# Optimization experiments

Measured on AMD Instinct MI355X. Metric: run time of the kernel, lower is better.

The kernel has to match this reference:

```python
import jax, jax.numpy as jnp
import numpy as np

D_MODEL = 512
NUM_HEADS = 8
HEAD_DIM = D_MODEL // NUM_HEADS
NUM_Z_BINS = 16
MAX_Z = 5.0
N = 2048


def setup_inputs() -> dict:
    key = jax.random.key(0)
    ks = jax.random.split(key, 12)
    s = 1.0 / np.sqrt(D_MODEL)
    return {
        "x": jax.random.normal(ks[0], (N, D_MODEL), dtype=jnp.float32),
        "z_matrix": jax.random.uniform(ks[1], (N, N), dtype=jnp.float32),
        "Wq": jax.random.normal(ks[2], (D_MODEL, D_MODEL), dtype=jnp.float32) * s,
        "bq": jnp.zeros((D_MODEL,), dtype=jnp.float32),
        "Wk": jax.random.normal(ks[3], (D_MODEL, D_MODEL), dtype=jnp.float32) * s,
        "bk": jnp.zeros((D_MODEL,), dtype=jnp.float32),
        "Wv": jax.random.normal(ks[4], (D_MODEL, D_MODEL), dtype=jnp.float32) * s,
        "bv": jnp.zeros((D_MODEL,), dtype=jnp.float32),
        "Wo": jax.random.normal(ks[5], (D_MODEL, D_MODEL), dtype=jnp.float32) * s,
        "bo": jnp.zeros((D_MODEL,), dtype=jnp.float32),
        "z_table": jax.random.normal(ks[6], (NUM_Z_BINS, NUM_HEADS), dtype=jnp.float32) * 0.02,
    }


def reference(x, z_matrix, Wq, bq, Wk, bk, Wv, bv, Wo, bo, z_table):
    n = x.shape[0]
    scale = HEAD_DIM ** -0.5
    q = (x @ Wq + bq).reshape(n, NUM_HEADS, HEAD_DIM)
    k = (x @ Wk + bk).reshape(n, NUM_HEADS, HEAD_DIM)
    v = (x @ Wv + bv).reshape(n, NUM_HEADS, HEAD_DIM)
    # [n, h, m] attention scores
    scores = jnp.einsum('nhd,mhd->nhm', q, k) * scale
    # Z-bus relative bias: bin pairwise z values into NUM_Z_BINS over [0, MAX_Z],
    # look up per-head bias from the embedding table.
    bins = jnp.clip(jnp.floor(z_matrix / MAX_Z * NUM_Z_BINS).astype(jnp.int32), 0, NUM_Z_BINS - 1)
    bias = z_table[bins]                    # [n, n, h]
    scores = scores + jnp.transpose(bias, (0, 2, 1))  # [n, h, n]
    attn = jax.nn.softmax(scores, axis=-1)  # dropout p=0.0 (eval)
    out = jnp.einsum('nhm,mhd->nhd', attn, v).reshape(n, D_MODEL)
    return out @ Wo + bo
```

## Files before the change

kernel.cpp:

```cpp
#include <hip/hip_runtime.h>


#define NTOK   2048
#define DM     512
#define NH     8
#define DH     64
#define NBINS  16
#define NSPLIT 4
#define KPS    (NTOK / NSPLIT)

typedef float  f32x16 __attribute__((ext_vector_type(16)));
typedef short  short8 __attribute__((ext_vector_type(8)));
typedef unsigned short ushort_t;

#define MFMA32(A, B, C) __builtin_amdgcn_mfma_f32_32x32x16_bf16((A), (B), (C), 0, 0, 0)

__device__ __forceinline__ unsigned short f2bf(float x) {
    union { float f; unsigned u; } v; v.f = x;
    unsigned r = v.u + 0x7FFFu + ((v.u >> 16) & 1u);
    return (unsigned short)(r >> 16);
}
__device__ __forceinline__ float bf2f(unsigned short b) {
    union { unsigned u; float f; } v; v.u = ((unsigned)b) << 16;
    return v.f;
}
__device__ __forceinline__ void splitbf(float x, unsigned short& hi, unsigned short& lo) {
    hi = f2bf(x);
    lo = f2bf(x - bf2f(hi));
}

union FragU { unsigned u[4]; short8 s; };

__device__ __forceinline__ int z_to_bin(float z) {
    int b = (int)floorf(z / 5.0f * 16.0f);
    return b < 0 ? 0 : (b > 15 ? 15 : b);
}

__global__ __launch_bounds__(256)
void bins_kernel(const float* __restrict__ z, unsigned char* __restrict__ bins) {
    int i = (blockIdx.x * 256 + threadIdx.x) * 4;
    float4 zv = *reinterpret_cast<const float4*>(z + i);
    uchar4 b;
    b.x = (unsigned char)z_to_bin(zv.x);
    b.y = (unsigned char)z_to_bin(zv.y);
    b.z = (unsigned char)z_to_bin(zv.z);
    b.w = (unsigned char)z_to_bin(zv.w);
    *reinterpret_cast<uchar4*>(bins + i) = b;
}

__global__ __launch_bounds__(256)
void prep_w(const float* __restrict__ Wq, const float* __restrict__ Wk,
            const float* __restrict__ Wv, const float* __restrict__ Wo,
            ushort_t* __restrict__ wt_hi_base, ushort_t* __restrict__ wt_lo_base) {
    const int z = blockIdx.z;
    const float* __restrict__ W = z == 0 ? Wq : z == 1 ? Wk : z == 2 ? Wv : Wo;
    ushort_t* __restrict__ th = wt_hi_base + (size_t)z * DM * DM * 2;
    ushort_t* __restrict__ tl = wt_lo_base + (size_t)z * DM * DM * 2;

    const int r0 = blockIdx.y * 32;
    const int c0 = blockIdx.x * 32;
    const int t  = threadIdx.x;

    __shared__ float Tl[32][33];

    {
        const int r = t >> 3, c4 = (t & 7) * 4;
        float4 v = *reinterpret_cast<const float4*>(W + (size_t)(r0 + r) * DM + c0 + c4);
        Tl[r][c4 + 0] = v.x; Tl[r][c4 + 1] = v.y; Tl[r][c4 + 2] = v.z; Tl[r][c4 + 3] = v.w;
    }
    __syncthreads();
    {
        const int c = t >> 3, r4 = (t & 7) * 4;
        ushort_t h4[4], l4[4];
        #pragma unroll
        for (int k = 0; k < 4; ++k) splitbf(Tl[r4 + k][c], h4[k], l4[k]);
        *reinterpret_cast<ushort4*>(th + (size_t)(c0 + c) * DM + r0 + r4) =
            make_ushort4(h4[0], h4[1], h4[2], h4[3]);
        *reinterpret_cast<ushort4*>(tl + (size_t)(c0 + c) * DM + r0 + r4) =
            make_ushort4(l4[0], l4[1], l4[2], l4[3]);
    }
}

__global__ __launch_bounds__(256)
void conv_x(const float* __restrict__ x, ushort_t* __restrict__ xh, ushort_t* __restrict__ xl) {
    int i = (blockIdx.x * 256 + threadIdx.x) * 4;
    float4 v = *reinterpret_cast<const float4*>(x + i);
    ushort_t h[4], l[4];
    splitbf(v.x, h[0], l[0]); splitbf(v.y, h[1], l[1]);
    splitbf(v.z, h[2], l[2]); splitbf(v.w, h[3], l[3]);
    *reinterpret_cast<ushort4*>(xh + i) = make_ushort4(h[0], h[1], h[2], h[3]);
    *reinterpret_cast<ushort4*>(xl + i) = make_ushort4(l[0], l[1], l[2], l[3]);
}

__global__ __launch_bounds__(256, 3)
void qkv_gemm_mfma(const ushort_t* __restrict__ x_hi, const ushort_t* __restrict__ x_lo,
                   const ushort_t* __restrict__ wqt_hi, const ushort_t* __restrict__ wqt_lo,
                   const ushort_t* __restrict__ wkt_hi, const ushort_t* __restrict__ wkt_lo,
                   const ushort_t* __restrict__ wvt_hi, const ushort_t* __restrict__ wvt_lo,
                   const float* __restrict__ bq, const float* __restrict__ bk,
                   const float* __restrict__ bv,
                   ushort_t* __restrict__ q_hi, ushort_t* __restrict__ q_lo,
                   ushort_t* __restrict__ k_hi, ushort_t* __restrict__ k_lo,
                   ushort_t* __restrict__ vT_hi, ushort_t* __restrict__ vT_lo) {
    const int z = blockIdx.z;
    const ushort_t* __restrict__ bt_hi = z == 0 ? wqt_hi : z == 1 ? wkt_hi : wvt_hi;
    const ushort_t* __restrict__ bt_lo = z == 0 ? wqt_lo : z == 1 ? wkt_lo : wvt_lo;
    const float*    __restrict__ bias  = z == 0 ? bq : z == 1 ? bk : bv;

    const int n0 = blockIdx.x * 64;
    const int m0 = blockIdx.y * 64;
    const int t  = threadIdx.x;
    const int wid = t >> 6, l = t & 63, hf = l >> 5, lq = l & 31;
    const int wm = wid >> 1, wn = wid & 1;

    __shared__ __align__(16) ushort_t Ash_hi[64 * 40], Ash_lo[64 * 40];
    __shared__ __align__(16) ushort_t Bsh_hi[64 * 40], Bsh_lo[64 * 40];

    f32x16 acc;
    #pragma unroll
    for (int i = 0; i < 16; ++i) acc[i] = 0.0f;

    const int sr = t >> 2, sc = t & 3;

    for (int k0 = 0; k0 < DM; k0 += 32) {
        __syncthreads();
        *reinterpret_cast<uint4*>(&Ash_hi[sr * 40 + 8 * sc]) =
            *reinterpret_cast<const uint4*>(&x_hi[(size_t)(m0 + sr) * DM + k0 + 8 * sc]);
        *reinterpret_cast<uint4*>(&Ash_lo[sr * 40 + 8 * sc]) =
            *reinterpret_cast<const uint4*>(&x_lo[(size_t)(m0 + sr) * DM + k0 + 8 * sc]);
        *reinterpret_cast<uint4*>(&Bsh_hi[sr * 40 + 8 * sc]) =
            *reinterpret_cast<const uint4*>(&bt_hi[(size_t)(n0 + sr) * DM + k0 + 8 * sc]);
        *reinterpret_cast<uint4*>(&Bsh_lo[sr * 40 + 8 * sc]) =
            *reinterpret_cast<const uint4*>(&bt_lo[(size_t)(n0 + sr) * DM + k0 + 8 * sc]);
        __syncthreads();

        #pragma unroll
        for (int kp = 0; kp < 2; ++kp) {
            const int co = 8 * (hf + 2 * kp);
            short8 ah = *reinterpret_cast<const short8*>(&Ash_hi[(32 * wm + lq) * 40 + co]);
            short8 al = *reinterpret_cast<const short8*>(&Ash_lo[(32 * wm + lq) * 40 + co]);
            short8 bh = *reinterpret_cast<const short8*>(&Bsh_hi[(32 * wn + lq) * 40 + co]);
            short8 bl = *reinterpret_cast<const short8*>(&Bsh_lo[(32 * wn + lq) * 40 + co]);
            acc = MFMA32(ah, bh, acc);
            acc = MFMA32(ah, bl, acc);
            acc = MFMA32(al, bh, acc);
        }
    }

    const int nl = lq + 32 * wn;
    const float bval = bias[n0 + nl];
    const int hh = n0 >> 6;

    #pragma unroll
    for (int r = 0; r < 16; ++r) {
        const int ml = (r & 3) + 8 * (r >> 2) + 4 * hf + 32 * wm;
        const float v = acc[r] + bval;
        ushort_t hi, lo; splitbf(v, hi, lo);
        if (z < 2) {
            ushort_t* dh = z == 0 ? q_hi : k_hi;
            ushort_t* dl = z == 0 ? q_lo : k_lo;
            const size_t o = ((size_t)hh * NTOK + m0 + ml) * DH + nl;
            dh[o] = hi; dl[o] = lo;
        } else {
            const size_t o = ((size_t)hh * DH + nl) * NTOK + m0 + ml;
            vT_hi[o] = hi; vT_lo[o] = lo;
        }
    }
}

__global__ __launch_bounds__(256, 3)
void wo_gemm_mfma(const ushort_t* __restrict__ a_hi, const ushort_t* __restrict__ a_lo,
                  const ushort_t* __restrict__ bt_hi, const ushort_t* __restrict__ bt_lo,
                  const float* __restrict__ bias, float* __restrict__ out) {
    const int n0 = blockIdx.x * 64;
    const int m0 = blockIdx.y * 64;
    const int t  = threadIdx.x;
    const int wid = t >> 6, l = t & 63, hf = l >> 5, lq = l & 31;
    const int wm = wid >> 1, wn = wid & 1;

    __shared__ __align__(16) ushort_t Ash_hi[64 * 40], Ash_lo[64 * 40];
    __shared__ __align__(16) ushort_t Bsh_hi[64 * 40], Bsh_lo[64 * 40];

    f32x16 acc;
    #pragma unroll
    for (int i = 0; i < 16; ++i) acc[i] = 0.0f;

    const int sr = t >> 2, sc = t & 3;

    for (int k0 = 0; k0 < DM; k0 += 32) {
        __syncthreads();
        *reinterpret_cast<uint4*>(&Ash_hi[sr * 40 + 8 * sc]) =
            *reinterpret_cast<const uint4*>(&a_hi[(size_t)(m0 + sr) * DM + k0 + 8 * sc]);
        *reinterpret_cast<uint4*>(&Ash_lo[sr * 40 + 8 * sc]) =
            *reinterpret_cast<const uint4*>(&a_lo[(size_t)(m0 + sr) * DM + k0 + 8 * sc]);
        *reinterpret_cast<uint4*>(&Bsh_hi[sr * 40 + 8 * sc]) =
            *reinterpret_cast<const uint4*>(&bt_hi[(size_t)(n0 + sr) * DM + k0 + 8 * sc]);
        *reinterpret_cast<uint4*>(&Bsh_lo[sr * 40 + 8 * sc]) =
            *reinterpret_cast<const uint4*>(&bt_lo[(size_t)(n0 + sr) * DM + k0 + 8 * sc]);
        __syncthreads();

        #pragma unroll
        for (int kp = 0; kp < 2; ++kp) {
            const int co = 8 * (hf + 2 * kp);
            short8 ah = *reinterpret_cast<const short8*>(&Ash_hi[(32 * wm + lq) * 40 + co]);
            short8 al = *reinterpret_cast<const short8*>(&Ash_lo[(32 * wm + lq) * 40 + co]);
            short8 bh = *reinterpret_cast<const short8*>(&Bsh_hi[(32 * wn + lq) * 40 + co]);
            short8 bl = *reinterpret_cast<const short8*>(&Bsh_lo[(32 * wn + lq) * 40 + co]);
            acc = MFMA32(ah, bh, acc);
            acc = MFMA32(ah, bl, acc);
            acc = MFMA32(al, bh, acc);
        }
    }

    const int nl = lq + 32 * wn;
    const float bval = bias[n0 + nl];
    #pragma unroll
    for (int r = 0; r < 16; ++r) {
        const int ml = (r & 3) + 8 * (r >> 2) + 4 * hf + 32 * wm;
        out[(size_t)(m0 + ml) * DM + n0 + nl] = acc[r] + bval;
    }
}

__global__ __launch_bounds__(256, 2)
void attn_mfma(const ushort_t* __restrict__ q_hi, const ushort_t* __restrict__ q_lo,
               const ushort_t* __restrict__ k_hi, const ushort_t* __restrict__ k_lo,
               const ushort_t* __restrict__ vT_hi, const ushort_t* __restrict__ vT_lo,
               const unsigned char* __restrict__ bins_g, const float* __restrict__ z_table,
               float* __restrict__ po, float* __restrict__ pm, float* __restrict__ pl) {
    const int hd = blockIdx.y;
    const int q0 = blockIdx.x * 128;
    const int zs = blockIdx.z;
    const int t  = threadIdx.x;
    const int wid = t >> 6, l = t & 63, hf = l >> 5, lq = l & 31;
    const int qs = q0 + 32 * wid;

    __shared__ __align__(16) ushort_t Ksh_hi[64 * 72], Ksh_lo[64 * 72];
    __shared__ __align__(16) ushort_t Vsh_hi[64 * 72], Vsh_lo[64 * 72];
    __shared__ __align__(16) unsigned char Bsh[128 * 80];

    const float ztab = z_table[(l & 15) * NH + hd];

    short8 qf_hi[4], qf_lo[4];
    #pragma unroll
    for (int kp = 0; kp < 4; ++kp) {
        const size_t o = ((size_t)hd * NTOK + qs + lq) * DH + 8 * hf + 16 * kp;
        qf_hi[kp] = *reinterpret_cast<const short8*>(&q_hi[o]);
        qf_lo[kp] = *reinterpret_cast<const short8*>(&q_lo[o]);
    }

    float m_run = -1e30f, l_run = 0.0f;
    f32x16 oacc0, oacc1;
    #pragma unroll
    for (int i = 0; i < 16; ++i) { oacc0[i] = 0.0f; oacc1[i] = 0.0f; }

    const float scale = 0.125f;
    const int kbase = zs * KPS;

    for (int kt8 = 0; kt8 < KPS / 64; ++kt8) {
        const int ktb = kbase + kt8 * 64;
        __syncthreads();
        #pragma unroll
        for (int i = 0; i < 2; ++i) {
            const int idx = t + 256 * i;
            const int r = idx >> 3, c = idx & 7;
            const size_t kg = ((size_t)hd * NTOK + ktb + r) * DH + 8 * c;
            const size_t vg = ((size_t)hd * DH + r) * NTOK + ktb + 8 * c;
            *reinterpret_cast<uint4*>(&Ksh_hi[r * 72 + 8 * c]) =
                *reinterpret_cast<const uint4*>(&k_hi[kg]);
            *reinterpret_cast<uint4*>(&Ksh_lo[r * 72 + 8 * c]) =
                *reinterpret_cast<const uint4*>(&k_lo[kg]);
            *reinterpret_cast<uint4*>(&Vsh_hi[r * 72 + 8 * c]) =
                *reinterpret_cast<const uint4*>(&vT_hi[vg]);
            *reinterpret_cast<uint4*>(&Vsh_lo[r * 72 + 8 * c]) =
                *reinterpret_cast<const uint4*>(&vT_lo[vg]);
        }
        #pragma unroll
        for (int i = 0; i < 2; ++i) {
            const int idx = t + 256 * i;
            const int qr = idx >> 2, c = idx & 3;
            *reinterpret_cast<uint4*>(&Bsh[qr * 80 + 16 * c]) =
                *reinterpret_cast<const uint4*>(&bins_g[(size_t)(q0 + qr) * NTOK + ktb + 16 * c]);
        }
        __syncthreads();

        f32x16 sacc0, sacc1;
        #pragma unroll
        for (int i = 0; i < 16; ++i) { sacc0[i] = 0.0f; sacc1[i] = 0.0f; }
        #pragma unroll
        for (int kp = 0; kp < 4; ++kp) {
            const int co = 8 * (hf + 2 * kp);
            short8 k0h = *reinterpret_cast<const short8*>(&Ksh_hi[lq * 72 + co]);
            short8 k0l = *reinterpret_cast<const short8*>(&Ksh_lo[lq * 72 + co]);
            short8 k1h = *reinterpret_cast<const short8*>(&Ksh_hi[(lq + 32) * 72 + co]);
            short8 k1l = *reinterpret_cast<const short8*>(&Ksh_lo[(lq + 32) * 72 + co]);
            sacc0 = MFMA32(k0h, qf_hi[kp], sacc0);
            sacc0 = MFMA32(k0h, qf_lo[kp], sacc0);
            sacc0 = MFMA32(k0l, qf_hi[kp], sacc0);
            sacc1 = MFMA32(k1h, qf_hi[kp], sacc1);
            sacc1 = MFMA32(k1h, qf_lo[kp], sacc1);
            sacc1 = MFMA32(k1l, qf_hi[kp], sacc1);
        }

        float sv[2][16];
        #pragma unroll
        for (int t2 = 0; t2 < 2; ++t2) {
            #pragma unroll
            for (int b = 0; b < 4; ++b) {
                const unsigned bw = *reinterpret_cast<const unsigned*>(
                    &Bsh[(32 * wid + lq) * 80 + 4 * (hf + 2 * b + 8 * t2)]);
                #pragma unroll
                for (int c = 0; c < 4; ++c) {
                    const int r = c + 4 * b;
                    const int src = (int)((bw >> (8 * c)) & 0xFF) | (l & 48);
                    const float bias = __shfl(ztab, src, 64);
                    const float sraw = (t2 == 0 ? sacc0[r] : sacc1[r]);
                    sv[t2][r] = sraw * scale + bias;
                }
            }
        }

        float tm = sv[0][0];
        #pragma unroll
        for (int t2 = 0; t2 < 2; ++t2)
            #pragma unroll
            for (int r = 0; r < 16; ++r) tm = fmaxf(tm, sv[t2][r]);
        tm = fmaxf(tm, __shfl_xor(tm, 32, 64));
        const float mn = fmaxf(m_run, tm);
        const float ef = __expf(m_run - mn);
        m_run = mn;

        float pv[2][16];
        float ts = 0.0f;
        #pragma unroll
        for (int t2 = 0; t2 < 2; ++t2)
            #pragma unroll
            for (int r = 0; r < 16; ++r) {
                const float p = __expf(sv[t2][r] - mn);
                pv[t2][r] = p;
                ts += p;
            }
        ts += __shfl_xor(ts, 32, 64);
        l_run = l_run * ef + ts;

        #pragma unroll
        for (int r = 0; r < 16; ++r) {
            const int qloc = (r & 3) + 8 * (r >> 2) + 4 * hf;
            const float efr = __shfl(ef, qloc | (l & 32), 64);
            oacc0[r] *= efr;
            oacc1[r] *= efr;
        }

        unsigned phi[2][8], plo[2][8];
        #pragma unroll
        for (int t2 = 0; t2 < 2; ++t2)
            #pragma unroll
            for (int i = 0; i < 8; ++i) {
                ushort_t ha, la, hb, lb;
                splitbf(pv[t2][2 * i],     ha, la);
                splitbf(pv[t2][2 * i + 1], hb, lb);
                phi[t2][i] = (unsigned)ha | ((unsigned)hb << 16);
                plo[t2][i] = (unsigned)la | ((unsigned)lb << 16);
            }

        FragU paf_hi[2][2], paf_lo[2][2];
        #pragma unroll
        for (int t2 = 0; t2 < 2; ++t2)
            #pragma unroll
            for (int e = 0; e < 2; ++e) {
                {
                    const unsigned pA0 = phi[t2][4 * e], pA1 = phi[t2][4 * e + 1];
                    const unsigned pB0 = phi[t2][4 * e + 2], pB1 = phi[t2][4 * e + 3];
                    const unsigned s0 = hf ? pA0 : pB0, s1 = hf ? pA1 : pB1;
                    const unsigned r0 = (unsigned)__shfl_xor((int)s0, 32, 64);
                    const unsigned r1 = (unsigned)__shfl_xor((int)s1, 32, 64);
                    paf_hi[t2][e].u[0] = hf ? r0 : pA0;
                    paf_hi[t2][e].u[1] = hf ? r1 : pA1;
                    paf_hi[t2][e].u[2] = hf ? pB0 : r0;
                    paf_hi[t2][e].u[3] = hf ? pB1 : r1;
                }
                {
                    const unsigned pA0 = plo[t2][4 * e], pA1 = plo[t2][4 * e + 1];
                    const unsigned pB0 = plo[t2][4 * e + 2], pB1 = plo[t2][4 * e + 3];
                    const unsigned s0 = hf ? pA0 : pB0, s1 = hf ? pA1 : pB1;
                    const unsigned r0 = (unsigned)__shfl_xor((int)s0, 32, 64);
                    const unsigned r1 = (unsigned)__shfl_xor((int)s1, 32, 64);
                    paf_lo[t2][e].u[0] = hf ? r0 : pA0;
                    paf_lo[t2][e].u[1] = hf ? r1 : pA1;
                    paf_lo[t2][e].u[2] = hf ? pB0 : r0;
                    paf_lo[t2][e].u[3] = hf ? pB1 : r1;
                }
            }

        #pragma unroll
        for (int kp = 0; kp < 4; ++kp) {
            const int t2 = kp >> 1, e = kp & 1;
            const int co = 8 * (hf + 2 * kp);
            short8 v0h = *reinterpret_cast<const short8*>(&Vsh_hi[lq * 72 + co]);
            short8 v0l = *reinterpret_cast<const short8*>(&Vsh_lo[lq * 72 + co]);
            oacc0 = MFMA32(paf_hi[t2][e].s, v0h, oacc0);
            oacc0 = MFMA32(paf_hi[t2][e].s, v0l, oacc0);
            oacc0 = MFMA32(paf_lo[t2][e].s, v0h, oacc0);
            short8 v1h = *reinterpret_cast<const short8*>(&Vsh_hi[(lq + 32) * 72 + co]);
            short8 v1l = *reinterpret_cast<const short8*>(&Vsh_lo[(lq + 32) * 72 + co]);
            oacc1 = MFMA32(paf_hi[t2][e].s, v1h, oacc1);
            oacc1 = MFMA32(paf_hi[t2][e].s, v1l, oacc1);
            oacc1 = MFMA32(paf_lo[t2][e].s, v1h, oacc1);
        }
    }

    #pragma unroll
    for (int r = 0; r < 16; ++r) {
        const int qloc = (r & 3) + 8 * (r >> 2) + 4 * hf;
        const size_t row = ((size_t)(zs * NH + hd) * NTOK + qs + qloc) * DH;
        po[row + lq]      = oacc0[r];
        po[row + lq + 32] = oacc1[r];
    }
    if (hf == 0) {
        const size_t row = (size_t)(zs * NH + hd) * NTOK + qs + lq;
        pm[row] = m_run;
        pl[row] = l_run;
    }
}

__global__ __launch_bounds__(256)
void merge_kernel(const float* __restrict__ po, const float* __restrict__ pm,
                  const float* __restrict__ pl,
                  ushort_t* __restrict__ o_hi, ushort_t* __restrict__ o_lo) {
    const int idx = blockIdx.x * 256 + threadIdx.x;
    const int d4 = (idx & 15) * 4;
    const int q  = (idx >> 4) & (NTOK - 1);
    const int hh = idx >> 15;

    float ms[NSPLIT];
    float M = -1e30f;
    #pragma unroll
    for (int s = 0; s < NSPLIT; ++s) {
        ms[s] = pm[((size_t)s * NH + hh) * NTOK + q];
        M = fmaxf(M, ms[s]);
    }
    float L = 0.0f;
    float4 o = make_float4(0.f, 0.f, 0.f, 0.f);
    #pragma unroll
    for (int s = 0; s < NSPLIT; ++s) {
        const float w = __expf(ms[s] - M);
        L += w * pl[((size_t)s * NH + hh) * NTOK + q];
        float4 p = *reinterpret_cast<const float4*>(
            po + (((size_t)s * NH + hh) * NTOK + q) * DH + d4);
        o.x += w * p.x; o.y += w * p.y; o.z += w * p.z; o.w += w * p.w;
    }
    const float inv = 1.0f / L;
    o.x *= inv; o.y *= inv; o.z *= inv; o.w *= inv;

    ushort_t h4[4], l4[4];
    splitbf(o.x, h4[0], l4[0]); splitbf(o.y, h4[1], l4[1]);
    splitbf(o.z, h4[2], l4[2]); splitbf(o.w, h4[3], l4[3]);
    const size_t oo = (size_t)q * DM + hh * DH + d4;
    *reinterpret_cast<ushort4*>(o_hi + oo) = make_ushort4(h4[0], h4[1], h4[2], h4[3]);
    *reinterpret_cast<ushort4*>(o_lo + oo) = make_ushort4(l4[0], l4[1], l4[2], l4[3]);
}

extern "C" void kernel_launch(void* const* d_in, const int* in_sizes, int n_in,
                              void* d_out, int out_size, void* d_ws, size_t ws_size,
                              hipStream_t stream) {
    const float* x        = (const float*)d_in[0];
    const float* z_matrix = (const float*)d_in[1];
    const float* Wq       = (const float*)d_in[2];
    const float* bq       = (const float*)d_in[3];
    const float* Wk       = (const float*)d_in[4];
    const float* bk       = (const float*)d_in[5];
    const float* Wv       = (const float*)d_in[6];
    const float* bv       = (const float*)d_in[7];
    const float* Wo       = (const float*)d_in[8];
    const float* bo       = (const float*)d_in[9];
    const float* z_table  = (const float*)d_in[10];
    float* out            = (float*)d_out;

    uint8_t* w = (uint8_t*)d_ws;
    const size_t MB = 1024 * 1024;
    ushort_t* x_hi  = (ushort_t*)(w + 0);
    ushort_t* x_lo  = (ushort_t*)(w + 2  * MB);
    ushort_t* wqt_hi= (ushort_t*)(w + 4  * MB);
    ushort_t* wqt_lo= (ushort_t*)(w + 4  * MB + 512 * 1024);
    ushort_t* wkt_hi= (ushort_t*)(w + 5  * MB);
    ushort_t* wkt_lo= (ushort_t*)(w + 5  * MB + 512 * 1024);
    ushort_t* wvt_hi= (ushort_t*)(w + 6  * MB);
    ushort_t* wvt_lo= (ushort_t*)(w + 6  * MB + 512 * 1024);
    ushort_t* wot_hi= (ushort_t*)(w + 7  * MB);
    ushort_t* wot_lo= (ushort_t*)(w + 7  * MB + 512 * 1024);
    ushort_t* q_hi  = (ushort_t*)(w + 8  * MB);
    ushort_t* q_lo  = (ushort_t*)(w + 10 * MB);
    ushort_t* k_hi  = (ushort_t*)(w + 12 * MB);
    ushort_t* k_lo  = (ushort_t*)(w + 14 * MB);
    ushort_t* vT_hi = (ushort_t*)(w + 16 * MB);
    ushort_t* vT_lo = (ushort_t*)(w + 18 * MB);
    unsigned char* bins = (unsigned char*)(w + 20 * MB);
    float* po = (float*)(w + 24 * MB);
    float* pm = (float*)(w + 40 * MB);
    float* pl = (float*)(w + 40 * MB + 256 * 1024);
    ushort_t* o_hi = x_hi;
    ushort_t* o_lo = x_lo;

    bins_kernel<<<dim3(NTOK * NTOK / 4 / 256), dim3(256), 0, stream>>>(z_matrix, bins);
    prep_w<<<dim3(16, 16, 4), dim3(256), 0, stream>>>(Wq, Wk, Wv, Wo,
        (ushort_t*)(w + 4 * MB), (ushort_t*)(w + 4 * MB + 512 * 1024));
    conv_x<<<dim3(NTOK * DM / 4 / 256), dim3(256), 0, stream>>>(x, x_hi, x_lo);

    qkv_gemm_mfma<<<dim3(DM / 64, NTOK / 64, 3), dim3(256), 0, stream>>>(
        x_hi, x_lo,
        wqt_hi, wqt_lo, wkt_hi, wkt_lo, wvt_hi, wvt_lo,
        bq, bk, bv,
        q_hi, q_lo, k_hi, k_lo, vT_hi, vT_lo);

    attn_mfma<<<dim3(NTOK / 128, NH, NSPLIT), dim3(256), 0, stream>>>(
        q_hi, q_lo, k_hi, k_lo, vT_hi, vT_lo, bins, z_table, po, pm, pl);

    merge_kernel<<<dim3(NH * NTOK * DH / 4 / 256), dim3(256), 0, stream>>>(
        po, pm, pl, o_hi, o_lo);

    wo_gemm_mfma<<<dim3(DM / 64, NTOK / 64), dim3(256), 0, stream>>>(
        o_hi, o_lo, wot_hi, wot_lo, bo, out);
}
```

Measured before the change: 174.5 us.

## Prefetch tiles into registers, merge prep kernels, raise MFMA priority

Three preprocessing kernels (z binning, x split, weight transpose/split) are merged into one launch to cut launch overhead. The QKV GEMM, Wo GEMM and attention kernels now load the next K-tile into registers while MFMAs run on the current LDS tile, so global-load latency overlaps compute. MFMA sections are wrapped in s_setprio to favour matrix issue. The manual bf16 rounding is replaced with the HIP intrinsic. The prefetch adds register pressure, which could lower occupancy, especially in the attention kernel.

```diff
diff --git a/kernel.cpp b/kernel.cpp
--- a/kernel.cpp
+++ b/kernel.cpp
@@ -1,4 +1,5 @@
 #include <hip/hip_runtime.h>
+#include <hip/hip_bf16.h>
 
 
 #define NTOK   2048
@@ -15,16 +16,16 @@
 
 #define MFMA32(A, B, C) __builtin_amdgcn_mfma_f32_32x32x16_bf16((A), (B), (C), 0, 0, 0)
 
-__device__ __forceinline__ unsigned short f2bf(float x) {
-    union { float f; unsigned u; } v; v.f = x;
-    unsigned r = v.u + 0x7FFFu + ((v.u >> 16) & 1u);
-    return (unsigned short)(r >> 16);
-}
-__device__ __forceinline__ float bf2f(unsigned short b) {
+__device__ __forceinline__ ushort_t f2bf(float x) {
+    __hip_bfloat16 h = __float2bfloat16(x);
+    union { __hip_bfloat16 b; ushort_t u; } v; v.b = h;
+    return v.u;
+}
+__device__ __forceinline__ float bf2f(ushort_t b) {
     union { unsigned u; float f; } v; v.u = ((unsigned)b) << 16;
     return v.f;
 }
-__device__ __forceinline__ void splitbf(float x, unsigned short& hi, unsigned short& lo) {
+__device__ __forceinline__ void splitbf(float x, ushort_t& hi, ushort_t& lo) {
     hi = f2bf(x);
     lo = f2bf(x - bf2f(hi));
 }
@@ -37,59 +38,58 @@
 }
 
 __global__ __launch_bounds__(256)
-void bins_kernel(const float* __restrict__ z, unsigned char* __restrict__ bins) {
-    int i = (blockIdx.x * 256 + threadIdx.x) * 4;
-    float4 zv = *reinterpret_cast<const float4*>(z + i);
-    uchar4 b;
-    b.x = (unsigned char)z_to_bin(zv.x);
-    b.y = (unsigned char)z_to_bin(zv.y);
-    b.z = (unsigned char)z_to_bin(zv.z);
-    b.w = (unsigned char)z_to_bin(zv.w);
-    *reinterpret_cast<uchar4*>(bins + i) = b;
-}
-
-__global__ __launch_bounds__(256)
-void prep_w(const float* __restrict__ Wq, const float* __restrict__ Wk,
-            const float* __restrict__ Wv, const float* __restrict__ Wo,
-            ushort_t* __restrict__ wt_hi_base, ushort_t* __restrict__ wt_lo_base) {
-    const int z = blockIdx.z;
-    const float* __restrict__ W = z == 0 ? Wq : z == 1 ? Wk : z == 2 ? Wv : Wo;
-    ushort_t* __restrict__ th = wt_hi_base + (size_t)z * DM * DM * 2;
-    ushort_t* __restrict__ tl = wt_lo_base + (size_t)z * DM * DM * 2;
-
-    const int r0 = blockIdx.y * 32;
-    const int c0 = blockIdx.x * 32;
-    const int t  = threadIdx.x;
-
+void prep_all(const float* __restrict__ z, unsigned char* __restrict__ bins,
+              const float* __restrict__ x, ushort_t* __restrict__ xh, ushort_t* __restrict__ xl,
+              const float* __restrict__ Wq, const float* __restrict__ Wk,
+              const float* __restrict__ Wv, const float* __restrict__ Wo,
+              ushort_t* __restrict__ wt_hi_base, ushort_t* __restrict__ wt_lo_base) {
+    const int bid = blockIdx.x;
+    const int t   = threadIdx.x;
     __shared__ float Tl[32][33];
 
-    {
-        const int r = t >> 3, c4 = (t & 7) * 4;
-        float4 v = *reinterpret_cast<const float4*>(W + (size_t)(r0 + r) * DM + c0 + c4);
-        Tl[r][c4 + 0] = v.x; Tl[r][c4 + 1] = v.y; Tl[r][c4 + 2] = v.z; Tl[r][c4 + 3] = v.w;
-    }
-    __syncthreads();
-    {
-        const int c = t >> 3, r4 = (t & 7) * 4;
-        ushort_t h4[4], l4[4];
-        #pragma unroll
-        for (int k = 0; k < 4; ++k) splitbf(Tl[r4 + k][c], h4[k], l4[k]);
-        *reinterpret_cast<ushort4*>(th + (size_t)(c0 + c) * DM + r0 + r4) =
-            make_ushort4(h4[0], h4[1], h4[2], h4[3]);
-        *reinterpret_cast<ushort4*>(tl + (size_t)(c0 + c) * DM + r0 + r4) =
-            make_ushort4(l4[0], l4[1], l4[2], l4[3]);
-    }
-}
-
-__global__ __launch_bounds__(256)
-void conv_x(const float* __restrict__ x, ushort_t* __restrict__ xh, ushort_t* __restrict__ xl) {
-    int i = (blockIdx.x * 256 + threadIdx.x) * 4;
-    float4 v = *reinterpret_cast<const float4*>(x + i);
-    ushort_t h[4], l[4];
-    splitbf(v.x, h[0], l[0]); splitbf(v.y, h[1], l[1]);
-    splitbf(v.z, h[2], l[2]); splitbf(v.w, h[3], l[3]);
-    *reinterpret_cast<ushort4*>(xh + i) = make_ushort4(h[0], h[1], h[2], h[3]);
-    *reinterpret_cast<ushort4*>(xl + i) = make_ushort4(l[0], l[1], l[2], l[3]);
+    if (bid < 4096) {
+        int i = (bid * 256 + t) * 4;
+        float4 zv = *reinterpret_cast<const float4*>(z + i);
+        uchar4 b;
+        b.x = (unsigned char)z_to_bin(zv.x);
+        b.y = (unsigned char)z_to_bin(zv.y);
+        b.z = (unsigned char)z_to_bin(zv.z);
+        b.w = (unsigned char)z_to_bin(zv.w);
+        *reinterpret_cast<uchar4*>(bins + i) = b;
+    } else if (bid < 5120) {
+        int i = ((bid - 4096) * 256 + t) * 4;
+        float4 v = *reinterpret_cast<const float4*>(x + i);
+        ushort_t h[4], l[4];
+        splitbf(v.x, h[0], l[0]); splitbf(v.y, h[1], l[1]);
+        splitbf(v.z, h[2], l[2]); splitbf(v.w, h[3], l[3]);
+        *reinterpret_cast<ushort4*>(xh + i) = make_ushort4(h[0], h[1], h[2], h[3]);
+        *reinterpret_cast<ushort4*>(xl + i) = make_ushort4(l[0], l[1], l[2], l[3]);
+    } else {
+        const int pz  = bid - 5120;
+        const int zz  = pz >> 8;
+        const int rem = pz & 255;
+        const float* __restrict__ W = zz == 0 ? Wq : zz == 1 ? Wk : zz == 2 ? Wv : Wo;
+        ushort_t* __restrict__ th = wt_hi_base + (size_t)zz * DM * DM * 2;
+        ushort_t* __restrict__ tl = wt_lo_base + (size_t)zz * DM * DM * 2;
+        const int r0 = (rem >> 4) * 32;
+        const int c0 = (rem & 15) * 32;
+        {
+            const int r = t >> 3, c4 = (t & 7) * 4;
+            float4 v = *reinterpret_cast<const float4*>(W + (size_t)(r0 + r) * DM + c0 + c4);
+            Tl[r][c4 + 0] = v.x; Tl[r][c4 + 1] = v.y; Tl[r][c4 + 2] = v.z; Tl[r][c4 + 3] = v.w;
+        }
+        __syncthreads();
+        {
+            const int c = t >> 3, r4 = (t & 7) * 4;
+            ushort_t h4[4], l4[4];
+            #pragma unroll
+            for (int k = 0; k < 4; ++k) splitbf(Tl[r4 + k][c], h4[k], l4[k]);
+            *reinterpret_cast<ushort4*>(th + (size_t)(c0 + c) * DM + r0 + r4) =
+                make_ushort4(h4[0], h4[1], h4[2], h4[3]);
+            *reinterpret_cast<ushort4*>(tl + (size_t)(c0 + c) * DM + r0 + r4) =
+                make_ushort4(l4[0], l4[1], l4[2], l4[3]);
+        }
+    }
 }
 
 __global__ __launch_bounds__(256, 3)
@@ -122,18 +122,25 @@
 
     const int sr = t >> 2, sc = t & 3;
 
+    uint4 ra_h, ra_l, rb_h, rb_l;
+    auto LOAD = [&](int k0) {
+        ra_h = *reinterpret_cast<const uint4*>(&x_hi[(size_t)(m0 + sr) * DM + k0 + 8 * sc]);
+        ra_l = *reinterpret_cast<const uint4*>(&x_lo[(size_t)(m0 + sr) * DM + k0 + 8 * sc]);
+        rb_h = *reinterpret_cast<const uint4*>(&bt_hi[(size_t)(n0 + sr) * DM + k0 + 8 * sc]);
+        rb_l = *reinterpret_cast<const uint4*>(&bt_lo[(size_t)(n0 + sr) * DM + k0 + 8 * sc]);
+    };
+    LOAD(0);
+
     for (int k0 = 0; k0 < DM; k0 += 32) {
         __syncthreads();
-        *reinterpret_cast<uint4*>(&Ash_hi[sr * 40 + 8 * sc]) =
-            *reinterpret_cast<const uint4*>(&x_hi[(size_t)(m0 + sr) * DM + k0 + 8 * sc]);
-        *reinterpret_cast<uint4*>(&Ash_lo[sr * 40 + 8 * sc]) =
-            *reinterpret_cast<const uint4*>(&x_lo[(size_t)(m0 + sr) * DM + k0 + 8 * sc]);
-        *reinterpret_cast<uint4*>(&Bsh_hi[sr * 40 + 8 * sc]) =
-            *reinterpret_cast<const uint4*>(&bt_hi[(size_t)(n0 + sr) * DM + k0 + 8 * sc]);
-        *reinterpret_cast<uint4*>(&Bsh_lo[sr * 40 + 8 * sc]) =
-            *reinterpret_cast<const uint4*>(&bt_lo[(size_t)(n0 + sr) * DM + k0 + 8 * sc]);
-        __syncthreads();
-
+        *reinterpret_cast<uint4*>(&Ash_hi[sr * 40 + 8 * sc]) = ra_h;
+        *reinterpret_cast<uint4*>(&Ash_lo[sr * 40 + 8 * sc]) = ra_l;
+        *reinterpret_cast<uint4*>(&Bsh_hi[sr * 40 + 8 * sc]) = rb_h;
+        *reinterpret_cast<uint4*>(&Bsh_lo[sr * 40 + 8 * sc]) = rb_l;
+        __syncthreads();
+        if (k0 + 32 < DM) LOAD(k0 + 32);
+
+        __builtin_amdgcn_s_setprio(1);
         #pragma unroll
         for (int kp = 0; kp < 2; ++kp) {
             const int co = 8 * (hf + 2 * kp);
@@ -145,6 +152,7 @@
             acc = MFMA32(ah, bl, acc);
             acc = MFMA32(al, bh, acc);
         }
+        __builtin_amdgcn_s_setprio(0);
     }
 
     const int nl = lq + 32 * wn;
@@ -187,18 +195,25 @@
 
     const int sr = t >> 2, sc = t & 3;
 
+    uint4 ra_h, ra_l, rb_h, rb_l;
+    auto LOAD = [&](int k0) {
+        ra_h = *reinterpret_cast<const uint4*>(&a_hi[(size_t)(m0 + sr) * DM + k0 + 8 * sc]);
+        ra_l = *reinterpret_cast<const uint4*>(&a_lo[(size_t)(m0 + sr) * DM + k0 + 8 * sc]);
+        rb_h = *reinterpret_cast<const uint4*>(&bt_hi[(size_t)(n0 + sr) * DM + k0 + 8 * sc]);
+        rb_l = *reinterpret_cast<const uint4*>(&bt_lo[(size_t)(n0 + sr) * DM + k0 + 8 * sc]);
+    };
+    LOAD(0);
+
     for (int k0 = 0; k0 < DM; k0 += 32) {
         __syncthreads();
-        *reinterpret_cast<uint4*>(&Ash_hi[sr * 40 + 8 * sc]) =
-            *reinterpret_cast<const uint4*>(&a_hi[(size_t)(m0 + sr) * DM + k0 + 8 * sc]);
-        *reinterpret_cast<uint4*>(&Ash_lo[sr * 40 + 8 * sc]) =
-            *reinterpret_cast<const uint4*>(&a_lo[(size_t)(m0 + sr) * DM + k0 + 8 * sc]);
-        *reinterpret_cast<uint4*>(&Bsh_hi[sr * 40 + 8 * sc]) =
-            *reinterpret_cast<const uint4*>(&bt_hi[(size_t)(n0 + sr) * DM + k0 + 8 * sc]);
-        *reinterpret_cast<uint4*>(&Bsh_lo[sr * 40 + 8 * sc]) =
-            *reinterpret_cast<const uint4*>(&bt_lo[(size_t)(n0 + sr) * DM + k0 + 8 * sc]);
-        __syncthreads();
-
+        *reinterpret_cast<uint4*>(&Ash_hi[sr * 40 + 8 * sc]) = ra_h;
+        *reinterpret_cast<uint4*>(&Ash_lo[sr * 40 + 8 * sc]) = ra_l;
+        *reinterpret_cast<uint4*>(&Bsh_hi[sr * 40 + 8 * sc]) = rb_h;
+        *reinterpret_cast<uint4*>(&Bsh_lo[sr * 40 + 8 * sc]) = rb_l;
+        __syncthreads();
+        if (k0 + 32 < DM) LOAD(k0 + 32);
+
+        __builtin_amdgcn_s_setprio(1);
         #pragma unroll
         for (int kp = 0; kp < 2; ++kp) {
             const int co = 8 * (hf + 2 * kp);
@@ -210,6 +225,7 @@
             acc = MFMA32(ah, bl, acc);
             acc = MFMA32(al, bh, acc);
         }
+        __builtin_amdgcn_s_setprio(0);
     }
 
     const int nl = lq + 32 * wn;
@@ -256,36 +272,52 @@
     const float scale = 0.125f;
     const int kbase = zs * KPS;
 
-    for (int kt8 = 0; kt8 < KPS / 64; ++kt8) {
-        const int ktb = kbase + kt8 * 64;
-        __syncthreads();
+    const int strow = t >> 3, stcol = (t & 7) * 8;
+    const int bqr = t >> 2, bcol = (t & 3) * 16;
+
+    uint4 rKh[2], rKl[2], rVh[2], rVl[2], rB[2];
+    auto LOADT = [&](int ktb) {
         #pragma unroll
         for (int i = 0; i < 2; ++i) {
-            const int idx = t + 256 * i;
-            const int r = idx >> 3, c = idx & 7;
-            const size_t kg = ((size_t)hd * NTOK + ktb + r) * DH + 8 * c;
-            const size_t vg = ((size_t)hd * DH + r) * NTOK + ktb + 8 * c;
-            *reinterpret_cast<uint4*>(&Ksh_hi[r * 72 + 8 * c]) =
-                *reinterpret_cast<const uint4*>(&k_hi[kg]);
-            *reinterpret_cast<uint4*>(&Ksh_lo[r * 72 + 8 * c]) =
-                *reinterpret_cast<const uint4*>(&k_lo[kg]);
-            *reinterpret_cast<uint4*>(&Vsh_hi[r * 72 + 8 * c]) =
-                *reinterpret_cast<const uint4*>(&vT_hi[vg]);
-            *reinterpret_cast<uint4*>(&Vsh_lo[r * 72 + 8 * c]) =
-                *reinterpret_cast<const uint4*>(&vT_lo[vg]);
+            const int r = strow + 32 * i;
+            const size_t kg = ((size_t)hd * NTOK + ktb + r) * DH + stcol;
+            const size_t vg = ((size_t)hd * DH + r) * NTOK + ktb + stcol;
+            rKh[i] = *reinterpret_cast<const uint4*>(&k_hi[kg]);
+            rKl[i] = *reinterpret_cast<const uint4*>(&k_lo[kg]);
+            rVh[i] = *reinterpret_cast<const uint4*>(&vT_hi[vg]);
+            rVl[i] = *reinterpret_cast<const uint4*>(&vT_lo[vg]);
         }
         #pragma unroll
         for (int i = 0; i < 2; ++i) {
-            const int idx = t + 256 * i;
-            const int qr = idx >> 2, c = idx & 3;
-            *reinterpret_cast<uint4*>(&Bsh[qr * 80 + 16 * c]) =
-                *reinterpret_cast<const uint4*>(&bins_g[(size_t)(q0 + qr) * NTOK + ktb + 16 * c]);
-        }
-        __syncthreads();
+            const int qr = bqr + 64 * i;
+            rB[i] = *reinterpret_cast<const uint4*>(&bins_g[(size_t)(q0 + qr) * NTOK + ktb + bcol]);
+        }
+    };
+    LOADT(kbase);
+
+    const int NT = KPS / 64;
+    for (int kt8 = 0; kt8 < NT; ++kt8) {
+        __syncthreads();
+        #pragma unroll
+        for (int i = 0; i < 2; ++i) {
+            const int r = strow + 32 * i;
+            *reinterpret_cast<uint4*>(&Ksh_hi[r * 72 + stcol]) = rKh[i];
+            *reinterpret_cast<uint4*>(&Ksh_lo[r * 72 + stcol]) = rKl[i];
+            *reinterpret_cast<uint4*>(&Vsh_hi[r * 72 + stcol]) = rVh[i];
+            *reinterpret_cast<uint4*>(&Vsh_lo[r * 72 + stcol]) = rVl[i];
+        }
+        #pragma unroll
+        for (int i = 0; i < 2; ++i) {
+            const int qr = bqr + 64 * i;
+            *reinterpret_cast<uint4*>(&Bsh[qr * 80 + bcol]) = rB[i];
+        }
+        __syncthreads();
+        if (kt8 + 1 < NT) LOADT(kbase + (kt8 + 1) * 64);
 
         f32x16 sacc0, sacc1;
         #pragma unroll
         for (int i = 0; i < 16; ++i) { sacc0[i] = 0.0f; sacc1[i] = 0.0f; }
+        __builtin_amdgcn_s_setprio(1);
         #pragma unroll
         for (int kp = 0; kp < 4; ++kp) {
             const int co = 8 * (hf + 2 * kp);
@@ -300,6 +332,7 @@
             sacc1 = MFMA32(k1h, qf_lo[kp], sacc1);
             sacc1 = MFMA32(k1l, qf_hi[kp], sacc1);
         }
+        __builtin_amdgcn_s_setprio(0);
 
         float sv[2][16];
         #pragma unroll
@@ -391,6 +424,7 @@
                 }
             }
 
+        __builtin_amdgcn_s_setprio(1);
         #pragma unroll
         for (int kp = 0; kp < 4; ++kp) {
             const int t2 = kp >> 1, e = kp & 1;
@@ -406,6 +440,7 @@
             oacc1 = MFMA32(paf_hi[t2][e].s, v1l, oacc1);
             oacc1 = MFMA32(paf_lo[t2][e].s, v1h, oacc1);
         }
+        __builtin_amdgcn_s_setprio(0);
     }
 
     #pragma unroll
@@ -500,10 +535,9 @@
     ushort_t* o_hi = x_hi;
     ushort_t* o_lo = x_lo;
 
-    bins_kernel<<<dim3(NTOK * NTOK / 4 / 256), dim3(256), 0, stream>>>(z_matrix, bins);
-    prep_w<<<dim3(16, 16, 4), dim3(256), 0, stream>>>(Wq, Wk, Wv, Wo,
+    prep_all<<<dim3(4096 + 1024 + 1024), dim3(256), 0, stream>>>(
+        z_matrix, bins, x, x_hi, x_lo, Wq, Wk, Wv, Wo,
         (ushort_t*)(w + 4 * MB), (ushort_t*)(w + 4 * MB + 512 * 1024));
-    conv_x<<<dim3(NTOK * DM / 4 / 256), dim3(256), 0, stream>>>(x, x_hi, x_lo);
 
     qkv_gemm_mfma<<<dim3(DM / 64, NTOK / 64, 3), dim3(256), 0, stream>>>(
         x_hi, x_lo,
```

Result: slower. 206.1 us (+18.1%).
